# Kernel optimization log

Measured on AMD Instinct MI355X. Metric: run time of the kernel, lower is better.

## Reference

```python
import jax, jax.numpy as jnp
import numpy as np

B, S, HID = 2, 2048, 2048
NH = 16
HD = HID // NH  # 128


def setup_inputs() -> dict:
    key = jax.random.key(0)
    ks = jax.random.split(key, 9)
    w = 0.02  # init scale to keep logits in a sane range
    return {
        "hidden_states": jax.random.normal(ks[0], (B, S, HID), dtype=jnp.float32),
        "Wq": jax.random.normal(ks[1], (HID, HID), dtype=jnp.float32) * w,
        "bq": jnp.zeros((HID,), dtype=jnp.float32),
        "Wk": jax.random.normal(ks[2], (HID, HD), dtype=jnp.float32) * w,
        "bk": jnp.zeros((HD,), dtype=jnp.float32),
        "Wv": jax.random.normal(ks[3], (HID, HD), dtype=jnp.float32) * w,
        "bv": jnp.zeros((HD,), dtype=jnp.float32),
        "Wo": jax.random.normal(ks[4], (HID, HID), dtype=jnp.float32) * w,
        "bo": jnp.zeros((HID,), dtype=jnp.float32),
    }


def reference(hidden_states, Wq, bq, Wk, bk, Wv, bv, Wo, bo):
    b, s, _ = hidden_states.shape
    # Projections (weights stored [in, out])
    q = hidden_states @ Wq + bq                      # [B,S,HID]
    k = hidden_states @ Wk + bk                      # [B,S,HD] single shared KV head
    v = hidden_states @ Wv + bv                      # [B,S,HD]
    q = q.reshape(b, s, NH, HD)                      # [B,S,H,D]
    # MQA: all query heads attend to the same K/V
    scores = jnp.einsum("bshd,btd->bhst", q, k) / jnp.sqrt(jnp.float32(HD))  # [B,H,S,S]
    probs = jax.nn.softmax(scores, axis=-1)
    attn = jnp.einsum("bhst,btd->bshd", probs, v)    # [B,S,H,D]
    attn = attn.reshape(b, s, HID)
    return attn @ Wo + bo
```

## Files before the change

kernel.cpp:

```cpp
#include <hip/hip_runtime.h>
#include <math.h>

#define BB  2
#define SS  2048
#define HID 2048
#define NH  16
#define HD  128
#define MT  (BB * SS)
#define NC  (HID + 2 * HD)
#define QK_SCALE 0.08838834764831845f

typedef unsigned short ushort_t;
typedef unsigned int uint_t;
typedef __bf16 bf16x8 __attribute__((ext_vector_type(8)));
typedef short short8 __attribute__((ext_vector_type(8)));
typedef float f32x4 __attribute__((ext_vector_type(4)));

__device__ __forceinline__ ushort_t f2bf(float x) {
    union { float f; uint_t u; } a; a.f = x;
    return (ushort_t)((a.u + 0x7FFFu + ((a.u >> 16) & 1u)) >> 16);
}
__device__ __forceinline__ ushort_t f2bf_fast(float x) {
    union { float f; uint_t u; } a; a.f = x;
    return (ushort_t)((a.u + 0x8000u) >> 16);
}

__device__ __forceinline__ int sw_addr(int r, int c) {
    return ((r >> 1) << 6) + ((((((r & 1) << 2) | c)) ^ ((r >> 1) & 7)) << 3);
}

#define CFENCE() asm volatile("" ::: "memory")

__global__ __launch_bounds__(256) void conv_bf16_kernel(
    const float* __restrict__ in, ushort_t* __restrict__ outb)
{
    const size_t i = ((size_t)blockIdx.x * 256 + threadIdx.x) * 8;
    const float4 a = *(const float4*)&in[i];
    const float4 b = *(const float4*)&in[i + 4];
    short8 o;
    o[0] = (short)f2bf(a.x); o[1] = (short)f2bf(a.y);
    o[2] = (short)f2bf(a.z); o[3] = (short)f2bf(a.w);
    o[4] = (short)f2bf(b.x); o[5] = (short)f2bf(b.y);
    o[6] = (short)f2bf(b.z); o[7] = (short)f2bf(b.w);
    *(short8*)&outb[i] = o;
}

__global__ __launch_bounds__(256) void convT_kernel(
    const float* __restrict__ W, ushort_t* __restrict__ Th, int K, int N)
{
    __shared__ float Ts[64][65];
    const int t = threadIdx.x;
    const int k0 = blockIdx.x * 64, n0 = blockIdx.y * 64;
    const int rr = t >> 4, c4 = (t & 15) * 4;
#pragma unroll
    for (int i = 0; i < 4; i++) {
        const int k = rr + i * 16;
        const float4 v = *(const float4*)&W[(size_t)(k0 + k) * N + n0 + c4];
        Ts[k][c4 + 0] = v.x; Ts[k][c4 + 1] = v.y;
        Ts[k][c4 + 2] = v.z; Ts[k][c4 + 3] = v.w;
    }
    __syncthreads();
    const int n = t >> 2, kc = (t & 3) * 16;
    short8 hv[2];
#pragma unroll
    for (int jj = 0; jj < 16; jj++)
        hv[jj >> 3][jj & 7] = (short)f2bf(Ts[kc + jj][n]);
    const size_t ob = (size_t)(n0 + n) * K + k0 + kc;
    *(short8*)&Th[ob]     = hv[0];
    *(short8*)&Th[ob + 8] = hv[1];
}

__global__ __launch_bounds__(256, 2) void gemm_qkv_kernel(
    const ushort_t* __restrict__ Ab, const ushort_t* __restrict__ WT,
    const float* __restrict__ bq, const float* __restrict__ bk,
    const float* __restrict__ bv,
    ushort_t* __restrict__ qb, ushort_t* __restrict__ kb,
    ushort_t* __restrict__ vtb)
{
    __shared__ short lds[8192];
    constexpr int AH = 0, BH = 4096;
    constexpr int K = HID;
    const int t  = threadIdx.x;
    const int wv = t >> 6, ln = t & 63;
    const int row0 = blockIdx.y * 128, col0 = blockIdx.x * 128;

    size_t agbase[2], bgbase[2];
    int    lbase[2];
#pragma unroll
    for (int i = 0; i < 2; i++) {
        const int I = wv * 2 + i;
        const int lrow = I * 8 + (ln >> 3);
        const int sb = (ln & 7) ^ (lrow & 7);
        const int rr = lrow * 2 + (sb >> 2);
        const int cc = sb & 3;
        agbase[i] = (size_t)(row0 + rr) * K + cc * 8;
        bgbase[i] = (size_t)(col0 + rr) * K + cc * 8;
        lbase[i] = I * 512;
    }

    const int wm0 = (wv & 1) * 64, wn0 = (wv >> 1) * 64;
    const int q = ln >> 4, lm = ln & 15;
    int aoff[4], boff[4];
#pragma unroll
    for (int i = 0; i < 4; i++) aoff[i] = sw_addr(wm0 + i * 16 + lm, q);
#pragma unroll
    for (int j = 0; j < 4; j++) boff[j] = sw_addr(wn0 + j * 16 + lm, q);

    f32x4 acc[4][4];
#pragma unroll
    for (int i = 0; i < 4; i++)
#pragma unroll
        for (int j = 0; j < 4; j++) acc[i][j] = 0.f;

    for (int k0 = 0; k0 < K; k0 += 32) {
        __syncthreads();
#pragma unroll
        for (int i = 0; i < 2; i++) {
            __builtin_amdgcn_global_load_lds(
                (const __attribute__((address_space(1))) void*)(Ab + agbase[i] + k0),
                (__attribute__((address_space(3))) void*)&lds[AH + lbase[i]], 16, 0, 0);
            __builtin_amdgcn_global_load_lds(
                (const __attribute__((address_space(1))) void*)(WT + bgbase[i] + k0),
                (__attribute__((address_space(3))) void*)&lds[BH + lbase[i]], 16, 0, 0);
        }
        __syncthreads();

        bf16x8 ah[4], bh[4];
#pragma unroll
        for (int i = 0; i < 4; i++) ah[i] = *(const bf16x8*)&lds[AH + aoff[i]];
#pragma unroll
        for (int j = 0; j < 4; j++) bh[j] = *(const bf16x8*)&lds[BH + boff[j]];
#pragma unroll
        for (int i = 0; i < 4; i++)
#pragma unroll
            for (int j = 0; j < 4; j++)
                acc[i][j] = __builtin_amdgcn_mfma_f32_16x16x32_bf16(ah[i], bh[j], acc[i][j], 0, 0, 0);
    }

    const int mode = (col0 < HID) ? 0 : ((col0 == HID) ? 1 : 2);
    const float* bsel = (mode == 0) ? bq : ((mode == 1) ? bk : bv);
    const int noff = (mode == 0) ? 0 : ((mode == 1) ? HID : HID + HD);
    float bj[4];
#pragma unroll
    for (int j = 0; j < 4; j++) bj[j] = bsel[col0 - noff + wn0 + j * 16 + lm];
#pragma unroll
    for (int i = 0; i < 4; i++) {
        const int mb = row0 + wm0 + i * 16 + q * 4;
#pragma unroll
        for (int j = 0; j < 4; j++) {
            const int nn = col0 + wn0 + j * 16 + lm;
#pragma unroll
            for (int rr2 = 0; rr2 < 4; rr2++) {
                const float v = acc[i][j][rr2] + bj[j];
                if (mode == 0)      qb [(size_t)(mb + rr2) * HID + nn]           = f2bf_fast(v * QK_SCALE);
                else if (mode == 1) kb [(size_t)(mb + rr2) * HD + (nn - HID)]    = f2bf_fast(v);
                else                vtb[(size_t)(nn - HID - HD) * MT + mb + rr2] = f2bf_fast(v);
            }
        }
    }
}

__global__ __launch_bounds__(256, 2) void gemm_oproj_kernel(
    const ushort_t* __restrict__ Ab, const ushort_t* __restrict__ WT,
    const float* __restrict__ bias, float* __restrict__ C, int M, int N, int K)
{
    __shared__ short lds[8192];
    constexpr int AH = 0, BH = 4096;
    const int t  = threadIdx.x;
    const int wv = t >> 6, ln = t & 63;
    const int row0 = blockIdx.y * 128, col0 = blockIdx.x * 128;

    size_t agbase[2], bgbase[2];
    int    lbase[2];
#pragma unroll
    for (int i = 0; i < 2; i++) {
        const int I = wv * 2 + i;
        const int lrow = I * 8 + (ln >> 3);
        const int sb = (ln & 7) ^ (lrow & 7);
        const int rr = lrow * 2 + (sb >> 2);
        const int cc = sb & 3;
        agbase[i] = (size_t)(row0 + rr) * K + cc * 8;
        bgbase[i] = (size_t)(col0 + rr) * K + cc * 8;
        lbase[i] = I * 512;
    }

    const int wm0 = (wv & 1) * 64, wn0 = (wv >> 1) * 64;
    const int q = ln >> 4, lm = ln & 15;
    int aoff[4], boff[4];
#pragma unroll
    for (int i = 0; i < 4; i++) aoff[i] = sw_addr(wm0 + i * 16 + lm, q);
#pragma unroll
    for (int j = 0; j < 4; j++) boff[j] = sw_addr(wn0 + j * 16 + lm, q);

    f32x4 acc[4][4];
#pragma unroll
    for (int i = 0; i < 4; i++)
#pragma unroll
        for (int j = 0; j < 4; j++) acc[i][j] = 0.f;

    for (int k0 = 0; k0 < K; k0 += 32) {
        __syncthreads();
#pragma unroll
        for (int i = 0; i < 2; i++) {
            __builtin_amdgcn_global_load_lds(
                (const __attribute__((address_space(1))) void*)(Ab + agbase[i] + k0),
                (__attribute__((address_space(3))) void*)&lds[AH + lbase[i]], 16, 0, 0);
            __builtin_amdgcn_global_load_lds(
                (const __attribute__((address_space(1))) void*)(WT + bgbase[i] + k0),
                (__attribute__((address_space(3))) void*)&lds[BH + lbase[i]], 16, 0, 0);
        }
        __syncthreads();

        bf16x8 ah[4], bh[4];
#pragma unroll
        for (int i = 0; i < 4; i++) ah[i] = *(const bf16x8*)&lds[AH + aoff[i]];
#pragma unroll
        for (int j = 0; j < 4; j++) bh[j] = *(const bf16x8*)&lds[BH + boff[j]];
#pragma unroll
        for (int i = 0; i < 4; i++)
#pragma unroll
            for (int j = 0; j < 4; j++)
                acc[i][j] = __builtin_amdgcn_mfma_f32_16x16x32_bf16(ah[i], bh[j], acc[i][j], 0, 0, 0);
    }

    float bj[4];
#pragma unroll
    for (int j = 0; j < 4; j++) bj[j] = bias[col0 + wn0 + j * 16 + lm];
#pragma unroll
    for (int i = 0; i < 4; i++) {
        const int mb = row0 + wm0 + i * 16 + q * 4;
#pragma unroll
        for (int j = 0; j < 4; j++) {
            const int nn = col0 + wn0 + j * 16 + lm;
#pragma unroll
            for (int rr2 = 0; rr2 < 4; rr2++)
                C[(size_t)(mb + rr2) * N + nn] = acc[i][j][rr2] + bj[j];
        }
    }
}

__global__ __launch_bounds__(256, 4) void attn_mfma_kernel(
    const ushort_t* __restrict__ qg, const ushort_t* __restrict__ kg,
    const ushort_t* __restrict__ vtg, ushort_t* Oh)
{
    __shared__ short Ks[8192], Vts[8192], Ps[4096];
    const int b = blockIdx.z, h = blockIdx.y, qt = blockIdx.x;
    const int t = threadIdx.x, wv = t >> 6, ln = t & 63;
    const int q = ln >> 4, lm = ln & 15;
    const int w16 = wv * 16;
    const int am = w16 + lm, amx = am & 15, amx7 = am & 7;

#pragma unroll
    for (int i = 0; i < 4; i++) {
        const int I = wv * 4 + i;
        const int r = 4 * I + (ln >> 4);
        const int c = (ln & 15) ^ (r & 15);
        const ushort_t* src = qg + (size_t)(b * SS + qt * 64 + r) * HID + h * HD + c * 8;
        __builtin_amdgcn_global_load_lds((const __attribute__((address_space(1))) void*)src,
            (__attribute__((address_space(3))) void*)&Ks[I * 512], 16, 0, 0);
    }
    __syncthreads();
    bf16x8 aq[4];
#pragma unroll
    for (int ks = 0; ks < 4; ks++)
        aq[ks] = *(const bf16x8*)&Ks[am * 128 + (((ks << 2) | q) ^ amx) * 8];
    __syncthreads();

    size_t kbase[4], vbase[4];
#pragma unroll
    for (int i = 0; i < 4; i++) {
        const int I = wv * 4 + i;
        { const int r = 4 * I + (ln >> 4); const int c = (ln & 15) ^ (r & 15);
          kbase[i] = (size_t)(b * SS + r) * HD + c * 8; }
        { const int r = 8 * I + (ln >> 3); const int c = (ln & 7) ^ (r & 7);
          vbase[i] = (size_t)r * MT + b * SS + c * 8; }
    }

#pragma unroll
    for (int i = 0; i < 4; i++) {
        const int I = wv * 4 + i;
        __builtin_amdgcn_global_load_lds(
            (const __attribute__((address_space(1))) void*)(kg + kbase[i]),
            (__attribute__((address_space(3))) void*)&Ks[I * 512], 16, 0, 0);
    }
#pragma unroll
    for (int i = 0; i < 4; i++) {
        const int I = wv * 4 + i;
        __builtin_amdgcn_global_load_lds(
            (const __attribute__((address_space(1))) void*)(vtg + vbase[i]),
            (__attribute__((address_space(3))) void*)&Vts[I * 512], 16, 0, 0);
    }

    float lrow[4] = {0.f, 0.f, 0.f, 0.f};
    f32x4 O[8];
#pragma unroll
    for (int ct = 0; ct < 8; ct++) O[ct] = 0.f;

    for (int kt = 0; kt < SS; kt += 64) {
        const int more = (kt + 64 < SS);

        asm volatile("s_waitcnt vmcnt(4)" ::: "memory");
        CFENCE();
        __builtin_amdgcn_s_barrier();
        CFENCE();

        f32x4 s[4];
#pragma unroll
        for (int ct = 0; ct < 4; ct++) s[ct] = 0.f;
        __builtin_amdgcn_s_setprio(1);
#pragma unroll
        for (int ks = 0; ks < 4; ks++) {
#pragma unroll
            for (int ct = 0; ct < 4; ct++) {
                const int n = ct * 16 + lm;
                const bf16x8 bk = *(const bf16x8*)&Ks[n * 128 + (((ks << 2) | q) ^ (n & 15)) * 8];
                s[ct] = __builtin_amdgcn_mfma_f32_16x16x32_bf16(aq[ks], bk, s[ct], 0, 0, 0);
            }
        }
        __builtin_amdgcn_s_setprio(0);

        CFENCE();
        __builtin_amdgcn_s_barrier();
        CFENCE();
        if (more) {
#pragma unroll
            for (int i = 0; i < 4; i++) {
                const int I = wv * 4 + i;
                __builtin_amdgcn_global_load_lds(
                    (const __attribute__((address_space(1))) void*)(kg + kbase[i] + (size_t)(kt + 64) * HD),
                    (__attribute__((address_space(3))) void*)&Ks[I * 512], 16, 0, 0);
            }
        }

#pragma unroll
        for (int ct = 0; ct < 4; ct++) {
            const int ch = ct * 2 + (lm >> 3);
#pragma unroll
            for (int r = 0; r < 4; r++) {
                const float p = __expf(s[ct][r]);
                lrow[r] += p;
                const int pr = w16 + q * 4 + r;
                Ps[pr * 64 + ((ch ^ (pr & 7)) << 3) + (lm & 7)] = (short)f2bf_fast(p);
            }
        }

        if (more) asm volatile("s_waitcnt vmcnt(4)" ::: "memory");
        else      asm volatile("s_waitcnt vmcnt(0)" ::: "memory");
        CFENCE();
        __builtin_amdgcn_s_barrier();
        CFENCE();

        __builtin_amdgcn_s_setprio(1);
#pragma unroll
        for (int ks = 0; ks < 2; ks++) {
            const bf16x8 ap = *(const bf16x8*)&Ps[am * 64 + (((ks << 2) | q) ^ amx7) * 8];
#pragma unroll
            for (int ct = 0; ct < 8; ct++) {
                const int d = ct * 16 + lm;
                const bf16x8 bv = *(const bf16x8*)&Vts[d * 64 + (((ks << 2) | q) ^ (d & 7)) * 8];
                O[ct] = __builtin_amdgcn_mfma_f32_16x16x32_bf16(ap, bv, O[ct], 0, 0, 0);
            }
        }
        __builtin_amdgcn_s_setprio(0);

        CFENCE();
        __builtin_amdgcn_s_barrier();
        CFENCE();
        if (more) {
#pragma unroll
            for (int i = 0; i < 4; i++) {
                const int I = wv * 4 + i;
                __builtin_amdgcn_global_load_lds(
                    (const __attribute__((address_space(1))) void*)(vtg + vbase[i] + kt + 64),
                    (__attribute__((address_space(3))) void*)&Vts[I * 512], 16, 0, 0);
            }
        }
    }

#pragma unroll
    for (int msk = 1; msk < 16; msk <<= 1)
#pragma unroll
        for (int r = 0; r < 4; r++) lrow[r] += __shfl_xor(lrow[r], msk);
#pragma unroll
    for (int r = 0; r < 4; r++) {
        const float inv = 1.f / lrow[r];
        const size_t base = (size_t)(b * SS + qt * 64 + w16 + q * 4 + r) * HID + h * HD;
#pragma unroll
        for (int ct = 0; ct < 8; ct++)
            Oh[base + ct * 16 + lm] = f2bf_fast(O[ct][r] * inv);
    }
}

extern "C" void kernel_launch(void* const* d_in, const int* in_sizes, int n_in,
                              void* d_out, int out_size, void* d_ws, size_t ws_size,
                              hipStream_t stream)
{
    const float* hs = (const float*)d_in[0];
    const float* Wq = (const float*)d_in[1];
    const float* bq = (const float*)d_in[2];
    const float* Wk = (const float*)d_in[3];
    const float* bk = (const float*)d_in[4];
    const float* Wv = (const float*)d_in[5];
    const float* bv = (const float*)d_in[6];
    const float* Wo = (const float*)d_in[7];
    const float* bo = (const float*)d_in[8];
    float* out = (float*)d_out;

    char* w = (char*)d_ws;
    ushort_t* hsb  = (ushort_t*)w;  w += (size_t)MT * HID * 2;
    ushort_t* qb   = (ushort_t*)w;  w += (size_t)MT * HID * 2;
    ushort_t* kb   = (ushort_t*)w;  w += (size_t)MT * HD * 2;
    ushort_t* vtb  = (ushort_t*)w;  w += (size_t)HD * MT * 2;
    ushort_t* WcT  = (ushort_t*)w;  w += (size_t)NC * HID * 2;
    ushort_t* WoT  = WcT;

    conv_bf16_kernel<<<(MT * HID) / (256 * 8), 256, 0, stream>>>(hs, hsb);
    convT_kernel<<<dim3(HID / 64, HID / 64), 256, 0, stream>>>(Wq, WcT, HID, HID);
    convT_kernel<<<dim3(HID / 64, HD / 64),  256, 0, stream>>>(
        Wk, WcT + (size_t)HID * HID, HID, HD);
    convT_kernel<<<dim3(HID / 64, HD / 64),  256, 0, stream>>>(
        Wv, WcT + (size_t)(HID + HD) * HID, HID, HD);

    gemm_qkv_kernel<<<dim3(NC / 128, MT / 128), 256, 0, stream>>>(
        hsb, WcT, bq, bk, bv, qb, kb, vtb);

    convT_kernel<<<dim3(HID / 64, HID / 64), 256, 0, stream>>>(Wo, WoT, HID, HID);

    attn_mfma_kernel<<<dim3(SS / 64, NH, BB), 256, 0, stream>>>(qb, kb, vtb, qb);

    gemm_oproj_kernel<<<dim3(HID / 128, MT / 128), 256, 0, stream>>>(
        qb, WoT, bo, out, MT, HID, HID);
}
```

Baseline: 324.9 us.

## Use two waves per attention block, each computing 32 query rows

The attention kernel now runs 128 threads (two waves) per block instead of four waves, and each wave handles two 16-row query subtiles. Each K and V fragment read from LDS feeds two MFMAs, which halves LDS read traffic per MFMA and raises the instruction-level parallelism inside each wave. Each thread issues twice as many async global-to-LDS loads, with the waitcnt thresholds adjusted to match. The cost is more registers per thread (doubled accumulators and query fragments) and fewer waves per block to hide latency, with launch bounds changed to (128,2).

```diff
diff --git a/kernel.cpp b/kernel.cpp
--- a/kernel.cpp
+++ b/kernel.cpp
@@ -239,7 +239,7 @@
     }
 }
 
-__global__ __launch_bounds__(256, 4) void attn_mfma_kernel(
+__global__ __launch_bounds__(128, 2) void attn_mfma_kernel(
     const ushort_t* __restrict__ qg, const ushort_t* __restrict__ kg,
     const ushort_t* __restrict__ vtg, ushort_t* Oh)
 {
@@ -247,66 +247,77 @@
     const int b = blockIdx.z, h = blockIdx.y, qt = blockIdx.x;
     const int t = threadIdx.x, wv = t >> 6, ln = t & 63;
     const int q = ln >> 4, lm = ln & 15;
-    const int w16 = wv * 16;
-    const int am = w16 + lm, amx = am & 15, amx7 = am & 7;
-
-#pragma unroll
-    for (int i = 0; i < 4; i++) {
-        const int I = wv * 4 + i;
+    const int w32 = wv * 32;
+    const int lm7 = ln & 7;
+
+    const ushort_t* qgb = qg + (size_t)(b * SS + qt * 64) * HID + h * HD;
+#pragma unroll
+    for (int i = 0; i < 8; i++) {
+        const int I = wv * 8 + i;
         const int r = 4 * I + (ln >> 4);
         const int c = (ln & 15) ^ (r & 15);
-        const ushort_t* src = qg + (size_t)(b * SS + qt * 64 + r) * HID + h * HD + c * 8;
-        __builtin_amdgcn_global_load_lds((const __attribute__((address_space(1))) void*)src,
+        __builtin_amdgcn_global_load_lds(
+            (const __attribute__((address_space(1))) void*)(qgb + (size_t)r * HID + c * 8),
             (__attribute__((address_space(3))) void*)&Ks[I * 512], 16, 0, 0);
     }
     __syncthreads();
-    bf16x8 aq[4];
-#pragma unroll
-    for (int ks = 0; ks < 4; ks++)
-        aq[ks] = *(const bf16x8*)&Ks[am * 128 + (((ks << 2) | q) ^ amx) * 8];
+    bf16x8 aq[2][4];
+#pragma unroll
+    for (int st = 0; st < 2; st++) {
+        const int am = w32 + st * 16 + lm;
+#pragma unroll
+        for (int ks = 0; ks < 4; ks++)
+            aq[st][ks] = *(const bf16x8*)&Ks[am * 128 + (((ks << 2) | q) ^ (am & 15)) * 8];
+    }
     __syncthreads();
 
-    size_t kbase[4], vbase[4];
-#pragma unroll
-    for (int i = 0; i < 4; i++) {
-        const int I = wv * 4 + i;
+    const ushort_t* kgb = kg + (size_t)b * SS * HD;
+    const ushort_t* vgb = vtg + b * SS;
+    uint_t koff[8], voff[8];
+#pragma unroll
+    for (int i = 0; i < 8; i++) {
+        const int I = wv * 8 + i;
         { const int r = 4 * I + (ln >> 4); const int c = (ln & 15) ^ (r & 15);
-          kbase[i] = (size_t)(b * SS + r) * HD + c * 8; }
+          koff[i] = (uint_t)(r * HD + c * 8); }
         { const int r = 8 * I + (ln >> 3); const int c = (ln & 7) ^ (r & 7);
-          vbase[i] = (size_t)r * MT + b * SS + c * 8; }
-    }
-
-#pragma unroll
-    for (int i = 0; i < 4; i++) {
-        const int I = wv * 4 + i;
+          voff[i] = (uint_t)(r * MT + c * 8); }
+    }
+
+#pragma unroll
+    for (int i = 0; i < 8; i++) {
+        const int I = wv * 8 + i;
         __builtin_amdgcn_global_load_lds(
-            (const __attribute__((address_space(1))) void*)(kg + kbase[i]),
+            (const __attribute__((address_space(1))) void*)(kgb + koff[i]),
             (__attribute__((address_space(3))) void*)&Ks[I * 512], 16, 0, 0);
     }
 #pragma unroll
-    for (int i = 0; i < 4; i++) {
-        const int I = wv * 4 + i;
+    for (int i = 0; i < 8; i++) {
+        const int I = wv * 8 + i;
         __builtin_amdgcn_global_load_lds(
-            (const __attribute__((address_space(1))) void*)(vtg + vbase[i]),
+            (const __attribute__((address_space(1))) void*)(vgb + voff[i]),
             (__attribute__((address_space(3))) void*)&Vts[I * 512], 16, 0, 0);
     }
 
-    float lrow[4] = {0.f, 0.f, 0.f, 0.f};
-    f32x4 O[8];
-#pragma unroll
-    for (int ct = 0; ct < 8; ct++) O[ct] = 0.f;
+    float lrow[2][4] = {{0.f, 0.f, 0.f, 0.f}, {0.f, 0.f, 0.f, 0.f}};
+    f32x4 O[2][8];
+#pragma unroll
+    for (int st = 0; st < 2; st++)
+#pragma unroll
+        for (int ct = 0; ct < 8; ct++) O[st][ct] = 0.f;
 
     for (int kt = 0; kt < SS; kt += 64) {
         const int more = (kt + 64 < SS);
 
-        asm volatile("s_waitcnt vmcnt(4)" ::: "memory");
+        asm volatile("s_waitcnt vmcnt(8)" ::: "memory");
         CFENCE();
         __builtin_amdgcn_s_barrier();
         CFENCE();
 
-        f32x4 s[4];
-#pragma unroll
-        for (int ct = 0; ct < 4; ct++) s[ct] = 0.f;
+        f32x4 s[2][4];
+#pragma unroll
+        for (int st = 0; st < 2; st++)
+#pragma unroll
+            for (int ct = 0; ct < 4; ct++) s[st][ct] = 0.f;
         __builtin_amdgcn_s_setprio(1);
 #pragma unroll
         for (int ks = 0; ks < 4; ks++) {
@@ -314,7 +325,8 @@
             for (int ct = 0; ct < 4; ct++) {
                 const int n = ct * 16 + lm;
                 const bf16x8 bk = *(const bf16x8*)&Ks[n * 128 + (((ks << 2) | q) ^ (n & 15)) * 8];
-                s[ct] = __builtin_amdgcn_mfma_f32_16x16x32_bf16(aq[ks], bk, s[ct], 0, 0, 0);
+                s[0][ct] = __builtin_amdgcn_mfma_f32_16x16x32_bf16(aq[0][ks], bk, s[0][ct], 0, 0, 0);
+                s[1][ct] = __builtin_amdgcn_mfma_f32_16x16x32_bf16(aq[1][ks], bk, s[1][ct], 0, 0, 0);
             }
         }
         __builtin_amdgcn_s_setprio(0);
@@ -324,27 +336,29 @@
         CFENCE();
         if (more) {
 #pragma unroll
-            for (int i = 0; i < 4; i++) {
-                const int I = wv * 4 + i;
+            for (int i = 0; i < 8; i++) {
+                const int I = wv * 8 + i;
                 __builtin_amdgcn_global_load_lds(
-                    (const __attribute__((address_space(1))) void*)(kg + kbase[i] + (size_t)(kt + 64) * HD),
+                    (const __attribute__((address_space(1))) void*)(kgb + koff[i] + (kt + 64) * HD),
                     (__attribute__((address_space(3))) void*)&Ks[I * 512], 16, 0, 0);
             }
         }
 
+#pragma unroll
+        for (int st = 0; st < 2; st++)
 #pragma unroll
         for (int ct = 0; ct < 4; ct++) {
             const int ch = ct * 2 + (lm >> 3);
 #pragma unroll
             for (int r = 0; r < 4; r++) {
-                const float p = __expf(s[ct][r]);
-                lrow[r] += p;
-                const int pr = w16 + q * 4 + r;
-                Ps[pr * 64 + ((ch ^ (pr & 7)) << 3) + (lm & 7)] = (short)f2bf_fast(p);
-            }
-        }
-
-        if (more) asm volatile("s_waitcnt vmcnt(4)" ::: "memory");
+                const float p = __expf(s[st][ct][r]);
+                lrow[st][r] += p;
+                const int pr = w32 + st * 16 + q * 4 + r;
+                Ps[pr * 64 + ((ch ^ (pr & 7)) << 3) + lm7] = (short)f2bf_fast(p);
+            }
+        }
+
+        if (more) asm volatile("s_waitcnt vmcnt(8)" ::: "memory");
         else      asm volatile("s_waitcnt vmcnt(0)" ::: "memory");
         CFENCE();
         __builtin_amdgcn_s_barrier();
@@ -353,12 +367,14 @@
         __builtin_amdgcn_s_setprio(1);
 #pragma unroll
         for (int ks = 0; ks < 2; ks++) {
-            const bf16x8 ap = *(const bf16x8*)&Ps[am * 64 + (((ks << 2) | q) ^ amx7) * 8];
+            const bf16x8 ap0 = *(const bf16x8*)&Ps[(w32 + lm) * 64 + (((ks << 2) | q) ^ lm7) * 8];
+            const bf16x8 ap1 = *(const bf16x8*)&Ps[(w32 + 16 + lm) * 64 + (((ks << 2) | q) ^ lm7) * 8];
 #pragma unroll
             for (int ct = 0; ct < 8; ct++) {
                 const int d = ct * 16 + lm;
                 const bf16x8 bv = *(const bf16x8*)&Vts[d * 64 + (((ks << 2) | q) ^ (d & 7)) * 8];
-                O[ct] = __builtin_amdgcn_mfma_f32_16x16x32_bf16(ap, bv, O[ct], 0, 0, 0);
+                O[0][ct] = __builtin_amdgcn_mfma_f32_16x16x32_bf16(ap0, bv, O[0][ct], 0, 0, 0);
+                O[1][ct] = __builtin_amdgcn_mfma_f32_16x16x32_bf16(ap1, bv, O[1][ct], 0, 0, 0);
             }
         }
         __builtin_amdgcn_s_setprio(0);
@@ -368,10 +384,10 @@
         CFENCE();
         if (more) {
 #pragma unroll
-            for (int i = 0; i < 4; i++) {
-                const int I = wv * 4 + i;
+            for (int i = 0; i < 8; i++) {
+                const int I = wv * 8 + i;
                 __builtin_amdgcn_global_load_lds(
-                    (const __attribute__((address_space(1))) void*)(vtg + vbase[i] + kt + 64),
+                    (const __attribute__((address_space(1))) void*)(vgb + voff[i] + (kt + 64)),
                     (__attribute__((address_space(3))) void*)&Vts[I * 512], 16, 0, 0);
             }
         }
@@ -380,14 +396,18 @@
 #pragma unroll
     for (int msk = 1; msk < 16; msk <<= 1)
 #pragma unroll
-        for (int r = 0; r < 4; r++) lrow[r] += __shfl_xor(lrow[r], msk);
+        for (int st = 0; st < 2; st++)
+#pragma unroll
+            for (int r = 0; r < 4; r++) lrow[st][r] += __shfl_xor(lrow[st][r], msk);
+#pragma unroll
+    for (int st = 0; st < 2; st++)
 #pragma unroll
     for (int r = 0; r < 4; r++) {
-        const float inv = 1.f / lrow[r];
-        const size_t base = (size_t)(b * SS + qt * 64 + w16 + q * 4 + r) * HID + h * HD;
+        const float inv = 1.f / lrow[st][r];
+        const size_t base = (size_t)(b * SS + qt * 64 + w32 + st * 16 + q * 4 + r) * HID + h * HD;
 #pragma unroll
         for (int ct = 0; ct < 8; ct++)
-            Oh[base + ct * 16 + lm] = f2bf_fast(O[ct][r] * inv);
+            Oh[base + ct * 16 + lm] = f2bf_fast(O[st][ct][r] * inv);
     }
 }
 
@@ -426,7 +446,7 @@
 
     convT_kernel<<<dim3(HID / 64, HID / 64), 256, 0, stream>>>(Wo, WoT, HID, HID);
 
-    attn_mfma_kernel<<<dim3(SS / 64, NH, BB), 256, 0, stream>>>(qb, kb, vtb, qb);
+    attn_mfma_kernel<<<dim3(SS / 64, NH, BB), 128, 0, stream>>>(qb, kb, vtb, qb);
 
     gemm_oproj_kernel<<<dim3(HID / 128, MT / 128), 256, 0, stream>>>(
         qb, WoT, bo, out, MT, HID, HID);
```

Result: no change. 322.0 us (-0.9%).
